# Optimization experiments

Hardware: AMD Instinct MI355X
Metric: run time of the kernel (lower is better)

## Reference

```python
import jax, jax.numpy as jnp
import numpy as np

EPS = 1e-06


def setup_inputs() -> dict:
    key = jax.random.key(0)
    k0, k1, k2, k3 = jax.random.split(key, 4)
    N = 4096  # num_gaussians (64**2)
    H = W = 128
    # Gaussian centers in [-1, 1]^2 (matches the init position grid range)
    position = jax.random.uniform(k0, (1, N, 2), minval=-1.0, maxval=1.0, dtype=jnp.float32)
    # Module stores color = raw_colors + 1 and subtracts 1 at the end of forward
    color = jax.random.uniform(k1, (1, N, 3), dtype=jnp.float32) + 1.0
    # Module init is log_scale = -5; use -3 +/- noise so kernels have visible support
    log_scale = jax.random.normal(k2, (1, N, 2), dtype=jnp.float32) * 0.5 - 3.0
    rotation = jax.random.normal(k3, (1, N), dtype=jnp.float32) * 0.5
    alphas = jnp.ones((1, N), dtype=jnp.float32)
    return dict(position=position, color=color, log_scale=log_scale,
                rotation=rotation, alphas=alphas, height=H, width=W, num_active=N)


def reference(position, color, log_scale, rotation, alphas, height, width, num_active):
    """2D anisotropic Gaussian splat render (dense per-pixel evaluation).

    For every pixel p and gaussian g: rotate the offset into the gaussian
    frame, evaluate exp(-0.5 * quadratic form), weight by alpha and
    accumulate color.  Output [1, 3, H, W] minus 1 (module returns render-1).
    """
    n = num_active
    pos = position[0, :n]                       # [N, 2]
    col = color[0, :n]                          # [N, 3]
    scale = jnp.exp(log_scale[0, :n]) + EPS     # [N, 2]
    rot = rotation[0, :n]                       # [N]
    alph = alphas[0, :n]                        # [N]

    # Pixel grid in [-1, 1], x along width, y along height
    xs = jnp.linspace(-1.0, 1.0, width, dtype=pos.dtype)
    ys = jnp.linspace(-1.0, 1.0, height, dtype=pos.dtype)
    x_grid, y_grid = jnp.meshgrid(xs, ys)       # each [H, W]
    P = height * width
    px = x_grid.reshape(P, 1)                   # [P, 1]
    py = y_grid.reshape(P, 1)

    dx = px - pos[None, :, 0]                   # [P, N]
    dy = py - pos[None, :, 1]                   # [P, N]
    c = jnp.cos(rot)[None, :]
    s = jnp.sin(rot)[None, :]
    u = dx * c + dy * s                         # rotated offsets [P, N]
    v = -dx * s + dy * c

    inv_sx = 1.0 / scale[:, 0][None, :]
    inv_sy = 1.0 / scale[:, 1][None, :]
    w = jnp.exp(-0.5 * ((u * inv_sx) ** 2 + (v * inv_sy) ** 2)) * alph[None, :]  # [P, N]

    img = jnp.einsum('pn,nc->pc', w, col)       # [P, 3]
    img = img.reshape(height, width, 3).transpose(2, 0, 1)[None]  # [1, 3, H, W]
    return img - 1.0
```

## Files before the change

### kernel.cpp

```cpp
#include <hip/hip_runtime.h>
#include <hip/hip_fp16.h>
#include <math.h>

#define EPSV 1e-6f
#define TPB 256
#define SLICES 32
#define PPT 4
#define GRP 2
#define GCAP 256

typedef float v2f __attribute__((ext_vector_type(2)));


__device__ __forceinline__ float pack_half2(float a, float b) {
    __half2 h = __floats2half2_rn(a, b);
    union { __half2 h; float f; } u; u.h = h;
    return u.f;
}

__global__ __launch_bounds__(TPB) void splat_fused(
        const float* __restrict__ pos,
        const float* __restrict__ col,
        const float* __restrict__ ls,
        const float* __restrict__ rot,
        const float* __restrict__ alph,
        const int* __restrict__ nact_p,
        const int* __restrict__ hptr,
        const int* __restrict__ wptr,
        float* __restrict__ partial,
        int N, int P, int g_per_slice) {
    __shared__ float4 sh[GCAP * 2];

    const int slice = blockIdx.y;
    const int t = threadIdx.x;

    int nact = *nact_p;
    for (int j = t; j < g_per_slice; j += TPB) {
        int g = slice * g_per_slice + j;
        float4 o0 = make_float4(0.f, 0.f, 0.f, 0.f);
        float4 o1 = o0;
        if (g < N && g < nact) {
            float sx = expf(ls[2 * g])     + EPSV;
            float sy = expf(ls[2 * g + 1]) + EPSV;
            float r  = rot[g];
            float c = cosf(r), s = sinf(r);
            const float K = 0.84932180028801904f;
            float iA =  K * c / sx;
            float iB =  K * s / sx;
            float iC = -K * s / sy;
            float iD =  K * c / sy;
            float px = pos[2 * g], py = pos[2 * g + 1];
            float E = -(iA * px + iB * py);
            float F = -(iC * px + iD * py);
            float a  = iA * iA + iC * iC;
            float b  = iB * iB + iD * iD;
            float cc = 2.0f * (iA * iB + iC * iD);
            float d  = 2.0f * (iA * E + iC * F);
            float e  = 2.0f * (iB * E + iD * F);
            float f  = E * E + F * F;
            float al = alph[g];
            float cr = al * col[3 * g];
            float cg = al * col[3 * g + 1];
            float cb = al * col[3 * g + 2];
            o0 = make_float4(-a, -b, -cc, -d);
            o1 = make_float4(-e, -f, pack_half2(cr, cg), pack_half2(cb, 0.f));
        }
        sh[2 * j]     = o0;
        sh[2 * j + 1] = o1;
    }
    __syncthreads();

    const int W = *wptr;
    const int H = *hptr;
    const int base = blockIdx.x * (TPB * PPT);
    v2f px2[GRP], py2[GRP], pxx2[GRP], pyy2[GRP], pxy2[GRP];
#pragma unroll
    for (int k = 0; k < GRP; ++k) {
#pragma unroll
        for (int e = 0; e < 2; ++e) {
            int p = base + t + (2 * k + e) * TPB;
            int x = (p < P) ? (p % W) : 0;
            int y = (p < P) ? (p / W) : 0;
            float fx = -1.0f + (float)x * (2.0f / (float)(W - 1));
            float fy = -1.0f + (float)y * (2.0f / (float)(H - 1));
            px2[k][e] = fx;  py2[k][e] = fy;
            pxx2[k][e] = fx * fx;  pyy2[k][e] = fy * fy;  pxy2[k][e] = fx * fy;
        }
    }

    v2f accr2[GRP], accg2[GRP], accb2[GRP];
#pragma unroll
    for (int k = 0; k < GRP; ++k) {
        accr2[k] = (v2f)(0.f); accg2[k] = (v2f)(0.f); accb2[k] = (v2f)(0.f);
    }

#pragma unroll 2
    for (int g = 0; g < g_per_slice; ++g) {
        float4 a0 = sh[2 * g];
        float4 a1 = sh[2 * g + 1];

        union { float f; __half2 h; } u01, u2x;
        u01.f = a1.z; u2x.f = a1.w;
        float cr = __low2float(u01.h);
        float cg = __high2float(u01.h);
        float cb = __low2float(u2x.h);

        v2f CA = {a0.x, a0.x}, CB = {a0.y, a0.y}, CC = {a0.z, a0.z};
        v2f CD = {a0.w, a0.w}, CE = {a1.x, a1.x}, CF = {a1.y, a1.y};
        v2f CR = {cr, cr}, CG = {cg, cg}, CBL = {cb, cb};

#pragma unroll
        for (int k = 0; k < GRP; ++k) {
            v2f tt = pxx2[k] * CA + CF;
            tt = pyy2[k] * CB + tt;
            tt = pxy2[k] * CC + tt;
            tt = px2[k]  * CD + tt;
            tt = py2[k]  * CE + tt;
            v2f w;
            w[0] = __builtin_amdgcn_exp2f(tt[0]);
            w[1] = __builtin_amdgcn_exp2f(tt[1]);
            accr2[k] = w * CR  + accr2[k];
            accg2[k] = w * CG  + accg2[k];
            accb2[k] = w * CBL + accb2[k];
        }
    }

    float* dst = partial + (size_t)slice * 3 * P;
#pragma unroll
    for (int k = 0; k < GRP; ++k) {
#pragma unroll
        for (int e = 0; e < 2; ++e) {
            int p = base + t + (2 * k + e) * TPB;
            if (p < P) {
                dst[p]         = accr2[k][e];
                dst[P + p]     = accg2[k][e];
                dst[2 * P + p] = accb2[k][e];
            }
        }
    }
}

__global__ __launch_bounds__(TPB) void splat_reduce(
        const float4* __restrict__ partial,
        float4* __restrict__ out,
        int total4) {
    int i = blockIdx.x * TPB + threadIdx.x;
    if (i >= total4) return;
    float4 s = make_float4(-1.f, -1.f, -1.f, -1.f);
#pragma unroll
    for (int sl = 0; sl < SLICES; ++sl) {
        float4 v = partial[(size_t)sl * total4 + i];
        s.x += v.x; s.y += v.y; s.z += v.z; s.w += v.w;
    }
    out[i] = s;
}

extern "C" void kernel_launch(void* const* d_in, const int* in_sizes, int n_in,
                              void* d_out, int out_size, void* d_ws, size_t ws_size,
                              hipStream_t stream) {
    const float* pos  = (const float*)d_in[0];
    const float* col  = (const float*)d_in[1];
    const float* ls   = (const float*)d_in[2];
    const float* rot  = (const float*)d_in[3];
    const float* alph = (const float*)d_in[4];
    const int*   hptr = (const int*)d_in[5];
    const int*   wptr = (const int*)d_in[6];
    const int*   nact = (const int*)d_in[7];

    int N = in_sizes[3];
    int P = out_size / 3;

    int g_per_slice = (N + SLICES - 1) / SLICES;
    if (g_per_slice > GCAP) g_per_slice = GCAP;

    float* partial = (float*)d_ws;

    int px_blocks = (P + TPB * PPT - 1) / (TPB * PPT);
    dim3 grid(px_blocks, SLICES);
    splat_fused<<<grid, TPB, 0, stream>>>(
        pos, col, ls, rot, alph, nact, hptr, wptr, partial, N, P, g_per_slice);

    int total4 = out_size / 4;
    splat_reduce<<<(total4 + TPB - 1) / TPB, TPB, 0, stream>>>(
        (const float4*)partial, (float4*)d_out, total4);
}
```

Before: 89.57 us.

## Cull gaussians per 32x32 pixel tile before the splat loop

```diff
diff --git a/kernel.cpp b/kernel.cpp
--- a/kernel.cpp
+++ b/kernel.cpp
@@ -8,6 +8,8 @@
 #define PPT 4
 #define GRP 2
 #define GCAP 256
+#define TILE 32
+#define CULL_R 5.5f
 
 typedef float v2f __attribute__((ext_vector_type(2)));
 
@@ -30,57 +32,94 @@
         float* __restrict__ partial,
         int N, int P, int g_per_slice) {
     __shared__ float4 sh[GCAP * 2];
+    __shared__ int s_cnt;
 
     const int slice = blockIdx.y;
     const int t = threadIdx.x;
+    const int W = *wptr;
+    const int H = *hptr;
+
+    const int ntx = (W + TILE - 1) / TILE;
+    const int nty = (H + TILE - 1) / TILE;
+    const bool use2d = (W > 1) && (H > 1) && (ntx * nty == (int)gridDim.x);
+
+    float bx0 = -1.f, bx1 = 1.f, by0 = -1.f, by1 = 1.f;
+    int tx = 0, ty = 0;
+    if (use2d) {
+        tx = blockIdx.x % ntx;
+        ty = blockIdx.x / ntx;
+        float iw = 2.0f / (float)(W - 1);
+        float ih = 2.0f / (float)(H - 1);
+        bx0 = -1.f + (float)(tx * TILE) * iw;
+        bx1 = -1.f + (float)min(tx * TILE + TILE - 1, W - 1) * iw;
+        by0 = -1.f + (float)(ty * TILE) * ih;
+        by1 = -1.f + (float)min(ty * TILE + TILE - 1, H - 1) * ih;
+    }
+
+    if (t == 0) s_cnt = 0;
+    __syncthreads();
 
     int nact = *nact_p;
     for (int j = t; j < g_per_slice; j += TPB) {
         int g = slice * g_per_slice + j;
-        float4 o0 = make_float4(0.f, 0.f, 0.f, 0.f);
-        float4 o1 = o0;
         if (g < N && g < nact) {
             float sx = expf(ls[2 * g])     + EPSV;
             float sy = expf(ls[2 * g + 1]) + EPSV;
-            float r  = rot[g];
-            float c = cosf(r), s = sinf(r);
-            const float K = 0.84932180028801904f;
-            float iA =  K * c / sx;
-            float iB =  K * s / sx;
-            float iC = -K * s / sy;
-            float iD =  K * c / sy;
-            float px = pos[2 * g], py = pos[2 * g + 1];
-            float E = -(iA * px + iB * py);
-            float F = -(iC * px + iD * py);
-            float a  = iA * iA + iC * iC;
-            float b  = iB * iB + iD * iD;
-            float cc = 2.0f * (iA * iB + iC * iD);
-            float d  = 2.0f * (iA * E + iC * F);
-            float e  = 2.0f * (iB * E + iD * F);
-            float f  = E * E + F * F;
-            float al = alph[g];
-            float cr = al * col[3 * g];
-            float cg = al * col[3 * g + 1];
-            float cb = al * col[3 * g + 2];
-            o0 = make_float4(-a, -b, -cc, -d);
-            o1 = make_float4(-e, -f, pack_half2(cr, cg), pack_half2(cb, 0.f));
-        }
-        sh[2 * j]     = o0;
-        sh[2 * j + 1] = o1;
+            float gx = pos[2 * g], gy = pos[2 * g + 1];
+            float R  = CULL_R * fmaxf(sx, sy);
+            float ddx = fminf(fmaxf(gx, bx0), bx1) - gx;
+            float ddy = fminf(fmaxf(gy, by0), by1) - gy;
+            if (ddx * ddx + ddy * ddy <= R * R) {
+                float r = rot[g];
+                float c = cosf(r), s = sinf(r);
+                const float K = 0.84932180028801904f;
+                float iA =  K * c / sx;
+                float iB =  K * s / sx;
+                float iC = -K * s / sy;
+                float iD =  K * c / sy;
+                float E = -(iA * gx + iB * gy);
+                float F = -(iC * gx + iD * gy);
+                float a  = iA * iA + iC * iC;
+                float b  = iB * iB + iD * iD;
+                float cc = 2.0f * (iA * iB + iC * iD);
+                float d  = 2.0f * (iA * E + iC * F);
+                float e  = 2.0f * (iB * E + iD * F);
+                float f  = E * E + F * F;
+                float al = alph[g];
+                float cr = al * col[3 * g];
+                float cg = al * col[3 * g + 1];
+                float cb = al * col[3 * g + 2];
+                int slot = atomicAdd(&s_cnt, 1);
+                sh[2 * slot]     = make_float4(-a, -b, -cc, -d);
+                sh[2 * slot + 1] = make_float4(-e, -f, pack_half2(cr, cg),
+                                               pack_half2(cb, 0.f));
+            }
+        }
     }
     __syncthreads();
-
-    const int W = *wptr;
-    const int H = *hptr;
+    const int m = s_cnt;
+
     const int base = blockIdx.x * (TPB * PPT);
     v2f px2[GRP], py2[GRP], pxx2[GRP], pyy2[GRP], pxy2[GRP];
+    int  pidx[GRP][2];
+    bool pact[GRP][2];
 #pragma unroll
     for (int k = 0; k < GRP; ++k) {
 #pragma unroll
         for (int e = 0; e < 2; ++e) {
-            int p = base + t + (2 * k + e) * TPB;
-            int x = (p < P) ? (p % W) : 0;
-            int y = (p < P) ? (p / W) : 0;
+            int x, y; bool act;
+            if (use2d) {
+                x = tx * TILE + (t & (TILE - 1));
+                y = ty * TILE + (t >> 5) + (2 * k + e) * (TPB / TILE);
+                act = (x < W) && (y < H);
+            } else {
+                int p = base + t + (2 * k + e) * TPB;
+                act = (p < P);
+                x = act ? (p % W) : 0;
+                y = act ? (p / W) : 0;
+            }
+            pidx[k][e] = y * W + x;
+            pact[k][e] = act;
             float fx = -1.0f + (float)x * (2.0f / (float)(W - 1));
             float fy = -1.0f + (float)y * (2.0f / (float)(H - 1));
             px2[k][e] = fx;  py2[k][e] = fy;
@@ -95,7 +134,7 @@
     }
 
 #pragma unroll 2
-    for (int g = 0; g < g_per_slice; ++g) {
+    for (int g = 0; g < m; ++g) {
         float4 a0 = sh[2 * g];
         float4 a1 = sh[2 * g + 1];
 
@@ -130,8 +169,8 @@
     for (int k = 0; k < GRP; ++k) {
 #pragma unroll
         for (int e = 0; e < 2; ++e) {
-            int p = base + t + (2 * k + e) * TPB;
-            if (p < P) {
+            if (pact[k][e]) {
+                int p = pidx[k][e];
                 dst[p]         = accr2[k][e];
                 dst[P + p]     = accg2[k][e];
                 dst[2 * P + p] = accb2[k][e];
```

Measured after the change: 80.64 us. -10.0%, faster.
